# Kernel tuning notes

Hardware: AMD Instinct MI355X
Metric: run time of the kernel (lower is better)

The kernel has to match this reference:

```python
import jax, jax.numpy as jnp
import numpy as np

VOCAB = 1_000_000
D = 128
N = 16384
NSAMP = 8192
TEMP = 0.05
L2_NORM = True


def _l2n(x):
    return x / (jnp.linalg.norm(x, axis=-1, keepdims=True) + 1e-12)


def setup_inputs() -> dict:
    key = jax.random.key(0)
    k1, k2, k3, k4, k5 = jax.random.split(key, 5)
    inputs = jax.random.normal(k1, (N, D), dtype=jnp.float32)
    target_ids = jax.random.randint(k2, (N, 1), 0, VOCAB, dtype=jnp.int64) if jax.config.jax_enable_x64 else jax.random.randint(k2, (N, 1), 0, VOCAB, dtype=jnp.int32)
    neg_ids = jax.random.randint(k3, (NSAMP,), 0, VOCAB, dtype=jnp.int32)
    weights = jax.random.uniform(k4, (N,), dtype=jnp.float32)
    projection = jax.random.normal(k5, (VOCAB, D), dtype=jnp.float32) * 0.02
    return {"inputs": inputs, "target_ids": target_ids, "neg_ids": neg_ids,
            "weights": weights, "projection": projection}


def reference(inputs, target_ids, neg_ids, weights, projection):
    # mask = (target_ids != -100).sum(-1).bool(); instead of dynamic boolean
    # indexing, fold the mask into the per-example weights (same weighted mean).
    valid = ((target_ids != -100).sum(axis=-1) > 0).astype(inputs.dtype)  # [N]
    tgt = jnp.clip(target_ids[:, 0], 0, VOCAB - 1)  # safe gather for masked rows

    pos_emb = projection[tgt]       # [N, D] gather
    neg_emb = projection[neg_ids]   # [S, D] gather

    x = inputs
    if L2_NORM:
        x = _l2n(x)
        pos_emb = _l2n(pos_emb)
        neg_emb = _l2n(neg_emb)

    pos_logit = jnp.einsum('nd,nd->n', x, pos_emb) / TEMP          # [N]
    neg_logits = jnp.einsum('nd,sd->ns', x, neg_emb) / TEMP        # [N, S]

    logits = jnp.concatenate([pos_logit[:, None], neg_logits], axis=-1)  # [N, 1+S]
    logZ = jax.scipy.special.logsumexp(logits, axis=-1)            # [N]
    ce = logZ - pos_logit                                          # -log p(pos)

    w = weights * valid
    loss = jnp.sum(ce * w) / jnp.maximum(jnp.sum(w), 1e-12)
    return loss
```

## Files before the change

### kernel.cpp

```cpp
#include <hip/hip_runtime.h>
#include <hip/hip_bf16.h>
#include <stdint.h>
#include <math.h>

#define VOCAB 1000000
#define D 128
#define NROWS 16384
#define NSAMP 8192
#define SSPLIT 16
#define K1F 28.853900817779268f
#define LOG2EF 1.4426950408889634f

#define XF_OFF 0u
#define EF_OFF 2097152u
#define PL_OFF 3145728u
#define SCX_OFF 3211264u
#define PS_OFF 3276800u
#define FP_OFF 4325376u
#define CNT_OFF 4326400u

typedef __attribute__((ext_vector_type(4))) int i32x4;
typedef __attribute__((ext_vector_type(16))) int i32x16;

#if __has_builtin(__builtin_amdgcn_exp2f)
#define EXP2(x) __builtin_amdgcn_exp2f(x)
#else
#define EXP2(x) exp2f(x)
#endif

__device__ __forceinline__ float wave_sum(float v) {
#pragma unroll
  for (int o = 1; o < 64; o <<= 1) v += __shfl_xor(v, o);
  return v;
}

__device__ __forceinline__ void store_frag_i8(char* __restrict__ base, int row,
                                              int lane, int bx, int by) {
  const int d = lane * 2;
  const int kk = d >> 5, sub = (d & 31) >> 4, j = d & 15;
  const int tile = row >> 5, lt = (sub << 5) | (row & 31);
  char* dst = base + (((size_t)(tile * 4 + kk) * 64 + lt) * 16 + j);
  dst[0] = (char)bx;
  dst[1] = (char)by;
}

__global__ __launch_bounds__(256) void prep_kernel(
    const float* __restrict__ x, const int* __restrict__ tgt,
    const int* __restrict__ nid, const float* __restrict__ proj,
    char* __restrict__ xf, char* __restrict__ ef,
    float* __restrict__ pl, float* __restrict__ scx,
    unsigned int* __restrict__ cnt) {
  if (blockIdx.x == 0 && threadIdx.x == 0) *cnt = 0u;
  const int wave = threadIdx.x >> 6, lane = threadIdx.x & 63;
  if (blockIdx.x < 1024) {
    const int n0 = blockIdx.x * 16 + wave * 4;
    int tg[4];
    float2 xr[4], pr[4];
#pragma unroll
    for (int i = 0; i < 4; ++i) {
      const int t = tgt[n0 + i];
      tg[i] = t < 0 ? 0 : (t > VOCAB - 1 ? VOCAB - 1 : t);
      xr[i] = *reinterpret_cast<const float2*>(x + (size_t)(n0 + i) * D + lane * 2);
    }
#pragma unroll
    for (int i = 0; i < 4; ++i)
      pr[i] = *reinterpret_cast<const float2*>(proj + (size_t)tg[i] * D + lane * 2);
#pragma unroll
    for (int i = 0; i < 4; ++i) {
      float sx = xr[i].x * xr[i].x + xr[i].y * xr[i].y;
      float sp = pr[i].x * pr[i].x + pr[i].y * pr[i].y;
      float dt = xr[i].x * pr[i].x + xr[i].y * pr[i].y;
      float mx = fmaxf(fabsf(xr[i].x), fabsf(xr[i].y));
#pragma unroll
      for (int o = 1; o < 64; o <<= 1) {
        sx += __shfl_xor(sx, o);
        sp += __shfl_xor(sp, o);
        dt += __shfl_xor(dt, o);
        mx = fmaxf(mx, __shfl_xor(mx, o));
      }
      const float norm = sqrtf(sx) + 1e-12f;
      if (lane == 0) {
        pl[n0 + i] = dt / (norm * (sqrtf(sp) + 1e-12f)) * 20.0f;
        scx[n0 + i] = K1F * (mx + 1e-20f) / (16129.0f * norm);
      }
      const float qs = 127.0f / (mx + 1e-20f);
      store_frag_i8(xf, n0 + i, lane, (int)rintf(xr[i].x * qs),
                    (int)rintf(xr[i].y * qs));
    }
  } else {
    const int s0 = (blockIdx.x - 1024) * 16 + wave * 4;
    float2 er[4];
#pragma unroll
    for (int i = 0; i < 4; ++i) {
      const int id = nid[s0 + i];
      er[i] = *reinterpret_cast<const float2*>(proj + (size_t)id * D + lane * 2);
    }
#pragma unroll
    for (int i = 0; i < 4; ++i) {
      const float qs =
          127.0f / (sqrtf(wave_sum(er[i].x * er[i].x + er[i].y * er[i].y)) + 1e-12f);
      store_frag_i8(ef, s0 + i, lane, (int)rintf(er[i].x * qs),
                    (int)rintf(er[i].y * qs));
    }
  }
}

#define LD16(p) (*reinterpret_cast<const i32x4*>(p))

#define PROC(A0_, A1_, A2_, A3_)                                             \
  do {                                                                       \
    i32x16 c0, c1;                                                           \
    _Pragma("unroll") for (int r = 0; r < 16; ++r) { c0[r] = 0; c1[r] = 0; } \
    c0 = __builtin_amdgcn_mfma_i32_32x32x32_i8(A0_, bq[0][0], c0, 0, 0, 0);  \
    c1 = __builtin_amdgcn_mfma_i32_32x32x32_i8(A0_, bq[1][0], c1, 0, 0, 0);  \
    c0 = __builtin_amdgcn_mfma_i32_32x32x32_i8(A1_, bq[0][1], c0, 0, 0, 0);  \
    c1 = __builtin_amdgcn_mfma_i32_32x32x32_i8(A1_, bq[1][1], c1, 0, 0, 0);  \
    c0 = __builtin_amdgcn_mfma_i32_32x32x32_i8(A2_, bq[0][2], c0, 0, 0, 0);  \
    c1 = __builtin_amdgcn_mfma_i32_32x32x32_i8(A2_, bq[1][2], c1, 0, 0, 0);  \
    c0 = __builtin_amdgcn_mfma_i32_32x32x32_i8(A3_, bq[0][3], c0, 0, 0, 0);  \
    c1 = __builtin_amdgcn_mfma_i32_32x32x32_i8(A3_, bq[1][3], c1, 0, 0, 0);  \
    _Pragma("unroll") for (int r = 0; r < 8; ++r) {                          \
      acc0a += EXP2((float)c0[2 * r] * scx0);                                \
      acc0b += EXP2((float)c0[2 * r + 1] * scx0);                            \
      acc1a += EXP2((float)c1[2 * r] * scx1);                                \
      acc1b += EXP2((float)c1[2 * r + 1] * scx1);                            \
    }                                                                        \
  } while (0)

__global__ __launch_bounds__(256, 4) void flash_kernel(
    const char* __restrict__ xf, const char* __restrict__ ef,
    const float* __restrict__ scx, float* __restrict__ psum) {
  const int tid = threadIdx.x, wave = tid >> 6, lane = tid & 63;
  const int nb = blockIdx.x & 63, ss = blockIdx.x >> 6;
  const int nbase = nb * 256 + wave * 64;

  i32x4 bq[2][4];
#pragma unroll
  for (int nf = 0; nf < 2; ++nf) {
    const char* p = xf + ((size_t)(nb * 8 + wave * 2 + nf) * 4096) + lane * 16;
#pragma unroll
    for (int kk = 0; kk < 4; ++kk)
      bq[nf][kk] = *reinterpret_cast<const i32x4*>(p + kk * 1024);
  }
  const float scx0 = scx[nbase + (lane & 31)];
  const float scx1 = scx[nbase + 32 + (lane & 31)];

  const char* esrc = ef + (size_t)ss * 65536 + lane * 16;
  float acc0a = 0.f, acc0b = 0.f, acc1a = 0.f, acc1b = 0.f;

  i32x4 A0 = LD16(esrc), A1 = LD16(esrc + 1024),
        A2 = LD16(esrc + 2048), A3 = LD16(esrc + 3072);
  i32x4 B0, B1, B2, B3;

#pragma unroll
  for (int t = 0; t < 16; t += 2) {
    {
      const char* p = esrc + (size_t)(t + 1) * 4096;
      B0 = LD16(p); B1 = LD16(p + 1024); B2 = LD16(p + 2048); B3 = LD16(p + 3072);
    }
    PROC(A0, A1, A2, A3);
    if (t + 2 < 16) {
      const char* p = esrc + (size_t)(t + 2) * 4096;
      A0 = LD16(p); A1 = LD16(p + 1024); A2 = LD16(p + 2048); A3 = LD16(p + 3072);
    }
    PROC(B0, B1, B2, B3);
  }

  float acc0 = acc0a + acc0b, acc1 = acc1a + acc1b;
  acc0 += __shfl_xor(acc0, 32);
  acc1 += __shfl_xor(acc1, 32);
  if (lane < 32) {
    psum[(size_t)ss * NROWS + nbase + lane] = acc0;
    psum[(size_t)ss * NROWS + nbase + 32 + lane] = acc1;
  }
}

__global__ __launch_bounds__(256) void finish_kernel(
    const float* __restrict__ psum, const float* __restrict__ pl,
    const int* __restrict__ tgt, const float* __restrict__ wts,
    float* __restrict__ fin, unsigned int* __restrict__ cnt,
    float* __restrict__ out) {
  const int n = blockIdx.x * 256 + threadIdx.x;
  float tot = 0.f;
#pragma unroll
  for (int s = 0; s < SSPLIT; ++s) tot += psum[(size_t)s * NROWS + n];
  const float p = pl[n];
  tot += EXP2(p * LOG2EF);
  const float ce = logf(tot) - p;
  const float w = wts[n] * (tgt[n] != -100 ? 1.f : 0.f);
  float a = wave_sum(ce * w);
  float b = wave_sum(w);
  __shared__ float sa[4], sb[4];
  __shared__ int last;
  const int wave = threadIdx.x >> 6, lane = threadIdx.x & 63;
  if (lane == 0) { sa[wave] = a; sb[wave] = b; }
  __syncthreads();
  if (threadIdx.x == 0) {
    __hip_atomic_store(&fin[blockIdx.x * 2], sa[0] + sa[1] + sa[2] + sa[3],
                       __ATOMIC_RELAXED, __HIP_MEMORY_SCOPE_AGENT);
    __hip_atomic_store(&fin[blockIdx.x * 2 + 1], sb[0] + sb[1] + sb[2] + sb[3],
                       __ATOMIC_RELAXED, __HIP_MEMORY_SCOPE_AGENT);
    const unsigned int old = __hip_atomic_fetch_add(cnt, 1u, __ATOMIC_ACQ_REL,
                                                    __HIP_MEMORY_SCOPE_AGENT);
    last = (old == 63u);
  }
  __syncthreads();
  if (last && threadIdx.x < 64) {
    const float A = wave_sum(__hip_atomic_load(&fin[threadIdx.x * 2],
                                               __ATOMIC_RELAXED,
                                               __HIP_MEMORY_SCOPE_AGENT));
    const float B = wave_sum(__hip_atomic_load(&fin[threadIdx.x * 2 + 1],
                                               __ATOMIC_RELAXED,
                                               __HIP_MEMORY_SCOPE_AGENT));
    if (threadIdx.x == 0) out[0] = A / fmaxf(B, 1e-12f);
  }
}

extern "C" void kernel_launch(void* const* d_in, const int* in_sizes, int n_in,
                              void* d_out, int out_size, void* d_ws, size_t ws_size,
                              hipStream_t stream) {
  const float* x    = (const float*)d_in[0];
  const int*   tgt  = (const int*)d_in[1];
  const int*   nid  = (const int*)d_in[2];
  const float* wts  = (const float*)d_in[3];
  const float* proj = (const float*)d_in[4];
  float* out = (float*)d_out;
  char* ws = (char*)d_ws;
  char* xf = ws + XF_OFF;
  char* ef = ws + EF_OFF;
  float* pl   = (float*)(ws + PL_OFF);
  float* scx  = (float*)(ws + SCX_OFF);
  float* psum = (float*)(ws + PS_OFF);
  float* fin  = (float*)(ws + FP_OFF);
  unsigned int* cnt = (unsigned int*)(ws + CNT_OFF);

  hipLaunchKernelGGL(prep_kernel, dim3(1024 + 512), dim3(256), 0, stream,
                     x, tgt, nid, proj, xf, ef, pl, scx, cnt);
  hipLaunchKernelGGL(flash_kernel, dim3(64 * SSPLIT), dim3(256), 0, stream,
                     xf, ef, scx, psum);
  hipLaunchKernelGGL(finish_kernel, dim3(NROWS / 256), dim3(256), 0, stream,
                     psum, pl, tgt, wts, fin, cnt, out);
}
```

Baseline: 41.59 us.

## Switch negative-logit GEMM from int8 to fp8 MFMA with prescaled operands

```diff
diff --git a/kernel.cpp b/kernel.cpp
--- a/kernel.cpp
+++ b/kernel.cpp
@@ -1,5 +1,6 @@
 #include <hip/hip_runtime.h>
 #include <hip/hip_bf16.h>
+#include <hip/hip_fp8.h>
 #include <stdint.h>
 #include <math.h>
 
@@ -14,13 +15,12 @@
 #define XF_OFF 0u
 #define EF_OFF 2097152u
 #define PL_OFF 3145728u
-#define SCX_OFF 3211264u
 #define PS_OFF 3276800u
 #define FP_OFF 4325376u
 #define CNT_OFF 4326400u
 
-typedef __attribute__((ext_vector_type(4))) int i32x4;
-typedef __attribute__((ext_vector_type(16))) int i32x16;
+typedef long long i64_t;
+typedef __attribute__((ext_vector_type(16))) float f32x16;
 
 #if __has_builtin(__builtin_amdgcn_exp2f)
 #define EXP2(x) __builtin_amdgcn_exp2f(x)
@@ -34,22 +34,31 @@
   return v;
 }
 
-__device__ __forceinline__ void store_frag_i8(char* __restrict__ base, int row,
-                                              int lane, int bx, int by) {
+__device__ __forceinline__ unsigned short to_fp8x2(float a, float b) {
+#if __has_builtin(__builtin_amdgcn_cvt_pk_fp8_f32)
+  const int p = __builtin_amdgcn_cvt_pk_fp8_f32(a, b, 0, false);
+  return (unsigned short)(p & 0xffff);
+#else
+  __hip_fp8_e4m3 fa(a), fb(b);
+  return (unsigned short)((unsigned)fa.__x | ((unsigned)fb.__x << 8));
+#endif
+}
+
+__device__ __forceinline__ void store_frag_fp8(unsigned char* __restrict__ base,
+                                               int row, int lane, float vx,
+                                               float vy) {
   const int d = lane * 2;
-  const int kk = d >> 5, sub = (d & 31) >> 4, j = d & 15;
+  const int kk = d >> 4, sub = (d & 15) >> 3, j = d & 7;
   const int tile = row >> 5, lt = (sub << 5) | (row & 31);
-  char* dst = base + (((size_t)(tile * 4 + kk) * 64 + lt) * 16 + j);
-  dst[0] = (char)bx;
-  dst[1] = (char)by;
+  unsigned char* dst = base + (((size_t)(tile * 8 + kk) * 64 + lt) * 8 + j);
+  *reinterpret_cast<unsigned short*>(dst) = to_fp8x2(vx, vy);
 }
 
 __global__ __launch_bounds__(256) void prep_kernel(
     const float* __restrict__ x, const int* __restrict__ tgt,
     const int* __restrict__ nid, const float* __restrict__ proj,
-    char* __restrict__ xf, char* __restrict__ ef,
-    float* __restrict__ pl, float* __restrict__ scx,
-    unsigned int* __restrict__ cnt) {
+    unsigned char* __restrict__ xf, unsigned char* __restrict__ ef,
+    float* __restrict__ pl, unsigned int* __restrict__ cnt) {
   if (blockIdx.x == 0 && threadIdx.x == 0) *cnt = 0u;
   const int wave = threadIdx.x >> 6, lane = threadIdx.x & 63;
   if (blockIdx.x < 1024) {
@@ -70,22 +79,17 @@
       float sx = xr[i].x * xr[i].x + xr[i].y * xr[i].y;
       float sp = pr[i].x * pr[i].x + pr[i].y * pr[i].y;
       float dt = xr[i].x * pr[i].x + xr[i].y * pr[i].y;
-      float mx = fmaxf(fabsf(xr[i].x), fabsf(xr[i].y));
 #pragma unroll
       for (int o = 1; o < 64; o <<= 1) {
         sx += __shfl_xor(sx, o);
         sp += __shfl_xor(sp, o);
         dt += __shfl_xor(dt, o);
-        mx = fmaxf(mx, __shfl_xor(mx, o));
       }
       const float norm = sqrtf(sx) + 1e-12f;
-      if (lane == 0) {
+      if (lane == 0)
         pl[n0 + i] = dt / (norm * (sqrtf(sp) + 1e-12f)) * 20.0f;
-        scx[n0 + i] = K1F * (mx + 1e-20f) / (16129.0f * norm);
-      }
-      const float qs = 127.0f / (mx + 1e-20f);
-      store_frag_i8(xf, n0 + i, lane, (int)rintf(xr[i].x * qs),
-                    (int)rintf(xr[i].y * qs));
+      const float sc = K1F / norm;
+      store_frag_fp8(xf, n0 + i, lane, xr[i].x * sc, xr[i].y * sc);
     }
   } else {
     const int s0 = (blockIdx.x - 1024) * 16 + wave * 4;
@@ -97,73 +101,70 @@
     }
 #pragma unroll
     for (int i = 0; i < 4; ++i) {
-      const float qs =
-          127.0f / (sqrtf(wave_sum(er[i].x * er[i].x + er[i].y * er[i].y)) + 1e-12f);
-      store_frag_i8(ef, s0 + i, lane, (int)rintf(er[i].x * qs),
-                    (int)rintf(er[i].y * qs));
-    }
-  }
-}
-
-#define LD16(p) (*reinterpret_cast<const i32x4*>(p))
-
-#define PROC(A0_, A1_, A2_, A3_)                                             \
-  do {                                                                       \
-    i32x16 c0, c1;                                                           \
-    _Pragma("unroll") for (int r = 0; r < 16; ++r) { c0[r] = 0; c1[r] = 0; } \
-    c0 = __builtin_amdgcn_mfma_i32_32x32x32_i8(A0_, bq[0][0], c0, 0, 0, 0);  \
-    c1 = __builtin_amdgcn_mfma_i32_32x32x32_i8(A0_, bq[1][0], c1, 0, 0, 0);  \
-    c0 = __builtin_amdgcn_mfma_i32_32x32x32_i8(A1_, bq[0][1], c0, 0, 0, 0);  \
-    c1 = __builtin_amdgcn_mfma_i32_32x32x32_i8(A1_, bq[1][1], c1, 0, 0, 0);  \
-    c0 = __builtin_amdgcn_mfma_i32_32x32x32_i8(A2_, bq[0][2], c0, 0, 0, 0);  \
-    c1 = __builtin_amdgcn_mfma_i32_32x32x32_i8(A2_, bq[1][2], c1, 0, 0, 0);  \
-    c0 = __builtin_amdgcn_mfma_i32_32x32x32_i8(A3_, bq[0][3], c0, 0, 0, 0);  \
-    c1 = __builtin_amdgcn_mfma_i32_32x32x32_i8(A3_, bq[1][3], c1, 0, 0, 0);  \
-    _Pragma("unroll") for (int r = 0; r < 8; ++r) {                          \
-      acc0a += EXP2((float)c0[2 * r] * scx0);                                \
-      acc0b += EXP2((float)c0[2 * r + 1] * scx0);                            \
-      acc1a += EXP2((float)c1[2 * r] * scx1);                                \
-      acc1b += EXP2((float)c1[2 * r + 1] * scx1);                            \
-    }                                                                        \
+      const float rn =
+          1.f / (sqrtf(wave_sum(er[i].x * er[i].x + er[i].y * er[i].y)) + 1e-12f);
+      store_frag_fp8(ef, s0 + i, lane, er[i].x * rn, er[i].y * rn);
+    }
+  }
+}
+
+#define LD8(p) (*reinterpret_cast<const i64_t*>(p))
+
+#define PROC(A_)                                                               \
+  do {                                                                         \
+    f32x16 c0, c1;                                                             \
+    _Pragma("unroll") for (int r = 0; r < 16; ++r) { c0[r] = 0.f; c1[r] = 0.f; } \
+    _Pragma("unroll") for (int kk = 0; kk < 8; ++kk) {                         \
+      c0 = __builtin_amdgcn_mfma_f32_32x32x16_fp8_fp8(A_[kk], bq[0][kk], c0,   \
+                                                      0, 0, 0);                \
+      c1 = __builtin_amdgcn_mfma_f32_32x32x16_fp8_fp8(A_[kk], bq[1][kk], c1,   \
+                                                      0, 0, 0);                \
+    }                                                                          \
+    _Pragma("unroll") for (int r = 0; r < 8; ++r) {                            \
+      acc0a += EXP2(c0[2 * r]);                                                \
+      acc0b += EXP2(c0[2 * r + 1]);                                            \
+      acc1a += EXP2(c1[2 * r]);                                                \
+      acc1b += EXP2(c1[2 * r + 1]);                                            \
+    }                                                                          \
   } while (0)
 
 __global__ __launch_bounds__(256, 4) void flash_kernel(
-    const char* __restrict__ xf, const char* __restrict__ ef,
-    const float* __restrict__ scx, float* __restrict__ psum) {
+    const unsigned char* __restrict__ xf, const unsigned char* __restrict__ ef,
+    float* __restrict__ psum) {
   const int tid = threadIdx.x, wave = tid >> 6, lane = tid & 63;
   const int nb = blockIdx.x & 63, ss = blockIdx.x >> 6;
   const int nbase = nb * 256 + wave * 64;
 
-  i32x4 bq[2][4];
+  i64_t bq[2][8];
 #pragma unroll
   for (int nf = 0; nf < 2; ++nf) {
-    const char* p = xf + ((size_t)(nb * 8 + wave * 2 + nf) * 4096) + lane * 16;
-#pragma unroll
-    for (int kk = 0; kk < 4; ++kk)
-      bq[nf][kk] = *reinterpret_cast<const i32x4*>(p + kk * 1024);
-  }
-  const float scx0 = scx[nbase + (lane & 31)];
-  const float scx1 = scx[nbase + 32 + (lane & 31)];
-
-  const char* esrc = ef + (size_t)ss * 65536 + lane * 16;
+    const unsigned char* p =
+        xf + ((size_t)(nb * 8 + wave * 2 + nf) * 4096) + lane * 8;
+#pragma unroll
+    for (int kk = 0; kk < 8; ++kk) bq[nf][kk] = LD8(p + kk * 512);
+  }
+
+  const unsigned char* esrc = ef + (size_t)ss * 65536 + lane * 8;
   float acc0a = 0.f, acc0b = 0.f, acc1a = 0.f, acc1b = 0.f;
 
-  i32x4 A0 = LD16(esrc), A1 = LD16(esrc + 1024),
-        A2 = LD16(esrc + 2048), A3 = LD16(esrc + 3072);
-  i32x4 B0, B1, B2, B3;
+  i64_t A[8], B[8];
+#pragma unroll
+  for (int kk = 0; kk < 8; ++kk) A[kk] = LD8(esrc + kk * 512);
 
 #pragma unroll
   for (int t = 0; t < 16; t += 2) {
     {
-      const char* p = esrc + (size_t)(t + 1) * 4096;
-      B0 = LD16(p); B1 = LD16(p + 1024); B2 = LD16(p + 2048); B3 = LD16(p + 3072);
-    }
-    PROC(A0, A1, A2, A3);
+      const unsigned char* p = esrc + (size_t)(t + 1) * 4096;
+#pragma unroll
+      for (int kk = 0; kk < 8; ++kk) B[kk] = LD8(p + kk * 512);
+    }
+    PROC(A);
     if (t + 2 < 16) {
-      const char* p = esrc + (size_t)(t + 2) * 4096;
-      A0 = LD16(p); A1 = LD16(p + 1024); A2 = LD16(p + 2048); A3 = LD16(p + 3072);
-    }
-    PROC(B0, B1, B2, B3);
+      const unsigned char* p = esrc + (size_t)(t + 2) * 4096;
+#pragma unroll
+      for (int kk = 0; kk < 8; ++kk) A[kk] = LD8(p + kk * 512);
+    }
+    PROC(B);
   }
 
   float acc0 = acc0a + acc0b, acc1 = acc1a + acc1b;
@@ -226,18 +227,17 @@
   const float* proj = (const float*)d_in[4];
   float* out = (float*)d_out;
   char* ws = (char*)d_ws;
-  char* xf = ws + XF_OFF;
-  char* ef = ws + EF_OFF;
+  unsigned char* xf = (unsigned char*)(ws + XF_OFF);
+  unsigned char* ef = (unsigned char*)(ws + EF_OFF);
   float* pl   = (float*)(ws + PL_OFF);
-  float* scx  = (float*)(ws + SCX_OFF);
   float* psum = (float*)(ws + PS_OFF);
   float* fin  = (float*)(ws + FP_OFF);
   unsigned int* cnt = (unsigned int*)(ws + CNT_OFF);
 
   hipLaunchKernelGGL(prep_kernel, dim3(1024 + 512), dim3(256), 0, stream,
-                     x, tgt, nid, proj, xf, ef, pl, scx, cnt);
+                     x, tgt, nid, proj, xf, ef, pl, cnt);
   hipLaunchKernelGGL(flash_kernel, dim3(64 * SSPLIT), dim3(256), 0, stream,
-                     xf, ef, scx, psum);
+                     xf, ef, psum);
   hipLaunchKernelGGL(finish_kernel, dim3(NROWS / 256), dim3(256), 0, stream,
                      psum, pl, tgt, wts, fin, cnt, out);
 }
```

After: 46.42 us. +11.6%, slower.
